# Optimization experiments

Hardware: AMD Instinct MI355X
Metric: run time of the kernel (lower is better)

Reference implementation:

```python
import jax, jax.numpy as jnp
import numpy as np

B, S, E, H, VS, VT = 128, 256, 512, 512, 32000, 32000


def _lstm_layer(x, mask, Wih, Whh, bih, bhh):
    # x: (S,B,E_in), mask: (S,B) bool. PyTorch gate order i,f,g,o.
    h0 = jnp.zeros((x.shape[1], Whh.shape[1]), x.dtype)
    c0 = h0
    def step(carry, inp):
        h, c = carry
        xt, mt = inp
        g = xt @ Wih.T + h @ Whh.T + bih + bhh
        i, f, gg, o = jnp.split(g, 4, axis=-1)
        i = jax.nn.sigmoid(i); f = jax.nn.sigmoid(f)
        gg = jnp.tanh(gg); o = jax.nn.sigmoid(o)
        c_new = f * c + i * gg
        h_new = o * jnp.tanh(c_new)
        m = mt[:, None]
        h2 = jnp.where(m, h_new, h)
        c2 = jnp.where(m, c_new, c)
        return (h2, c2), jnp.where(m, h_new, 0.0)  # pad_packed zero-pads
    (hT, cT), ys = jax.lax.scan(step, (h0, c0), (x, mask))
    return ys, cT


def setup_inputs() -> dict:
    key = jax.random.key(0)
    ks = jax.random.split(key, 32)
    def w(k, shape, fan_in):
        bound = 1.0 / np.sqrt(fan_in)
        return jax.random.uniform(k, shape, jnp.float32, -bound, bound)
    src_tokens = jax.random.randint(ks[0], (B, S), 0, VS)
    src_lens = jnp.sort(jax.random.randint(ks[1], (B,), S // 2, S + 1))[::-1]
    src_lens = src_lens.at[0].set(S)  # pack_padded expects descending, max = S
    trg_tokens = jax.random.randint(ks[2], (B,), 0, VT)
    inp = {
        'src_tokens': src_tokens, 'src_lens': src_lens, 'trg_tokens': trg_tokens,
        'src_emb': jax.random.normal(ks[3], (VS, E), jnp.float32),
        'trg_emb': jax.random.normal(ks[4], (VT, E), jnp.float32),
        'enc_Wih0': w(ks[5], (4 * H, E), H), 'enc_Whh0': w(ks[6], (4 * H, H), H),
        'enc_bih0': w(ks[7], (4 * H,), H), 'enc_bhh0': w(ks[8], (4 * H,), H),
        'enc_Wih1': w(ks[9], (4 * H, H), H), 'enc_Whh1': w(ks[10], (4 * H, H), H),
        'enc_bih1': w(ks[11], (4 * H,), H), 'enc_bhh1': w(ks[12], (4 * H,), H),
        'dec_Wih': w(ks[13], (4 * H, E + H), H), 'dec_Whh': w(ks[14], (4 * H, H), H),
        'dec_bih': w(ks[15], (4 * H,), H), 'dec_bhh': w(ks[16], (4 * H,), H),
        'W_init': w(ks[17], (H, 2 * H), 2 * H), 'b_init': w(ks[18], (H,), 2 * H),
        'W_hid': w(ks[19], (H, 2 * H), 2 * H), 'b_hid': w(ks[20], (H,), 2 * H),
        'W_out': w(ks[21], (VT, H), H), 'b_out': w(ks[22], (VT,), H),
    }
    return inp


def reference(src_tokens, src_lens, trg_tokens, src_emb, trg_emb,
              enc_Wih0, enc_Whh0, enc_bih0, enc_bhh0,
              enc_Wih1, enc_Whh1, enc_bih1, enc_bhh1,
              dec_Wih, dec_Whh, dec_bih, dec_bhh,
              W_init, b_init, W_hid, b_hid, W_out, b_out):
    # ---- encode ----
    x = src_emb[src_tokens]                       # (B,S,E)
    x = jnp.transpose(x, (1, 0, 2))               # (S,B,E)
    mask = jnp.arange(S)[:, None] < src_lens[None, :]  # (S,B)
    y0, c0f = _lstm_layer(x, mask, enc_Wih0, enc_Whh0, enc_bih0, enc_bhh0)
    y1, c1f = _lstm_layer(y0, mask, enc_Wih1, enc_Whh1, enc_bih1, enc_bhh1)
    src_states = jnp.transpose(y1, (1, 0, 2))     # (B,S,H)
    # final cell states (num_layers,B,H) -> (B, num_layers*H)
    final_cells = jnp.concatenate([c0f, c1f], axis=-1)  # (B,2H)
    c_dec = final_cells @ W_init.T + b_init       # (B,H)
    h_dec = jnp.tanh(c_dec)
    # ---- one decoder step ----
    emb_t = trg_emb[trg_tokens]                   # (B,E)
    vec = jnp.concatenate([emb_t, jnp.zeros((B, H), emb_t.dtype)], axis=-1)
    g = vec @ dec_Wih.T + h_dec @ dec_Whh.T + dec_bih + dec_bhh
    i, f, gg, o = jnp.split(g, 4, axis=-1)
    c = jax.nn.sigmoid(f) * c_dec + jax.nn.sigmoid(i) * jnp.tanh(gg)
    h = jax.nn.sigmoid(o) * jnp.tanh(c)           # (B,H)
    # ---- masked dot attention ----
    scores = jnp.einsum('bsh,bh->bs', src_states, h)
    smask = jnp.arange(S)[None, :] < src_lens[:, None]
    scores = jnp.where(smask, scores, -jnp.inf)
    attw = jax.nn.softmax(scores, axis=-1)
    context = jnp.einsum('bs,bsh->bh', attw, src_states)
    attn_vec = jnp.concatenate([h, context], axis=-1) @ W_hid.T + b_hid
    logits = attn_vec @ W_out.T + b_out
    prd_token = jnp.argmax(logits, axis=-1)       # softmax is monotone
    return context, h, prd_token
```

## Files before the change

### kernel.cpp

```cpp
#include <hip/hip_runtime.h>
#include <stdint.h>


typedef _Float16 f16;
typedef f16 f16x8 __attribute__((ext_vector_type(8)));
typedef float f32x4 __attribute__((ext_vector_type(4)));

#define LOSCALE 2048.0f
#define LOINV   (1.0f/2048.0f)

#define B_  128
#define S_  256
#define H_  512

__device__ __forceinline__ uint16_t hbits(f16 h){ union{ f16 f; uint16_t u; } c; c.f=h; return c.u; }

__device__ __forceinline__ uint32_t split_ph2(float x){
  f16 h = (f16)x;
  float r = (x - (float)h) * LOSCALE;
  return (uint32_t)hbits(h) | ((uint32_t)hbits((f16)r) << 16);
}
__device__ __forceinline__ float ph2val(uint32_t p){
  union{ uint16_t u; f16 f; } a, b; a.u = (uint16_t)p; b.u = (uint16_t)(p>>16);
  return (float)a.f + (float)b.f * LOINV;
}

__device__ __forceinline__ void pack_hi_lo(const uint4& a, const uint4& b, uint4& hi, uint4& lo){
  hi = make_uint4((a.x & 0xffffu) | (a.y << 16),
                  (a.z & 0xffffu) | (a.w << 16),
                  (b.x & 0xffffu) | (b.y << 16),
                  (b.z & 0xffffu) | (b.w << 16));
  lo = make_uint4((a.x >> 16) | (a.y & 0xffff0000u),
                  (a.z >> 16) | (a.w & 0xffff0000u),
                  (b.x >> 16) | (b.y & 0xffff0000u),
                  (b.z >> 16) | (b.w & 0xffff0000u));
}

__device__ __forceinline__ void split_pack8(const float* x, uint4& hi, uint4& lo){
  uint16_t h[8], l[8];
#pragma unroll
  for (int e = 0; e < 8; ++e) {
    f16 hh = (f16)x[e];
    float r = (x[e] - (float)hh) * LOSCALE;
    h[e] = hbits(hh); l[e] = hbits((f16)r);
  }
  hi = make_uint4((uint32_t)h[0]|((uint32_t)h[1]<<16), (uint32_t)h[2]|((uint32_t)h[3]<<16),
                  (uint32_t)h[4]|((uint32_t)h[5]<<16), (uint32_t)h[6]|((uint32_t)h[7]<<16));
  lo = make_uint4((uint32_t)l[0]|((uint32_t)l[1]<<16), (uint32_t)l[2]|((uint32_t)l[3]<<16),
                  (uint32_t)l[4]|((uint32_t)l[5]<<16), (uint32_t)l[6]|((uint32_t)l[7]<<16));
}

__device__ __forceinline__ f32x4 mfma16(uint4 a, uint4 b, f32x4 c){
  return __builtin_amdgcn_mfma_f32_16x16x32_f16(
      __builtin_bit_cast(f16x8, a), __builtin_bit_cast(f16x8, b), c, 0, 0, 0);
}

__device__ __forceinline__ float sigm(float x){ return 1.0f/(1.0f + expf(-x)); }
__device__ __forceinline__ float fsigm(float x){ return 1.0f/(1.0f + __expf(-x)); }
__device__ __forceinline__ float ftanh(float x){
  float ax = fabsf(x);
  float e = __expf(-2.0f*ax);
  float r = (1.0f - e)/(1.0f + e);
  return copysignf(r, x);
}

__global__ __launch_bounds__(256) void k_embed_src(const int* __restrict__ tok,
    const float* __restrict__ emb, uint32_t* __restrict__ out)
{
  const size_t total = (size_t)S_ * B_ * H_;
  for (size_t i = (size_t)blockIdx.x*256 + threadIdx.x; i < total; i += (size_t)gridDim.x*256) {
    int e = (int)(i & (H_-1)); int row = (int)(i >> 9);
    int b = row & (B_-1), s = row >> 7;
    int t = tok[b*S_ + s];
    out[i] = split_ph2(emb[(size_t)t*H_ + e]);
  }
}

__global__ __launch_bounds__(256) void k_embed_trg(const int* __restrict__ tok,
    const float* __restrict__ emb, uint32_t* __restrict__ out)
{
  int i = blockIdx.x*256 + threadIdx.x;
  int e = i & (H_-1), b = i >> 9;
  int t = tok[b];
  out[i] = split_ph2(emb[(size_t)t*H_ + e]);
}

__global__ __launch_bounds__(256,2) void k_gemm(
    const uint32_t* __restrict__ A, int lda,
    const void* __restrict__ W, int ldw, int bsplit,
    const float* __restrict__ b0, const float* __restrict__ b1,
    float* __restrict__ C, int N, int K, int addC)
{
  __shared__ uint8_t sm[65536];
  const int tid = threadIdx.x;
  const int lane = tid & 63, wv = tid >> 6;
  const int wm = wv >> 1, wn = wv & 1;
  const int bn0 = blockIdx.x * 128, bm0 = blockIdx.y * 128;

  const int srow = tid >> 1;
  const int skh  = (tid & 1) * 32;
  const int smt  = srow >> 4, sr = srow & 15, skt = tid & 1;

  f32x4 acc0[4][4], acc1[4][4];
#pragma unroll
  for (int i = 0; i < 4; ++i)
#pragma unroll
    for (int j = 0; j < 4; ++j) { acc0[i][j] = (f32x4){0,0,0,0}; acc1[i][j] = (f32x4){0,0,0,0}; }

  for (int k0 = 0; k0 < K; k0 += 64) {
    __syncthreads();
    {
      const uint32_t* ap = A + (size_t)(bm0 + srow) * lda + (k0 + skh);
      uint4 q[8];
#pragma unroll
      for (int e = 0; e < 8; ++e) q[e] = *(const uint4*)(ap + e*4);
#pragma unroll
      for (int kg = 0; kg < 4; ++kg) {
        uint4 hi, lo; pack_hi_lo(q[2*kg], q[2*kg+1], hi, lo);
        uint8_t* dst = sm + (size_t)(smt*2 + skt)*2048 + (size_t)(sr + 16*kg)*16;
        *(uint4*)dst = hi; *(uint4*)(dst + 1024) = lo;
      }
    }
    if (bsplit) {
      const uint32_t* wp = (const uint32_t*)W + (size_t)(bn0 + srow) * ldw + (k0 + skh);
      uint4 q[8];
#pragma unroll
      for (int e = 0; e < 8; ++e) q[e] = *(const uint4*)(wp + e*4);
#pragma unroll
      for (int kg = 0; kg < 4; ++kg) {
        uint4 hi, lo; pack_hi_lo(q[2*kg], q[2*kg+1], hi, lo);
        uint8_t* dst = sm + 32768 + (size_t)(smt*2 + skt)*2048 + (size_t)(sr + 16*kg)*16;
        *(uint4*)dst = hi; *(uint4*)(dst + 1024) = lo;
      }
    } else {
      const float* wp = (const float*)W + (size_t)(bn0 + srow) * ldw + (k0 + skh);
      float xs[32];
#pragma unroll
      for (int e = 0; e < 8; ++e) { float4 v = *(const float4*)(wp + e*4);
        xs[e*4+0]=v.x; xs[e*4+1]=v.y; xs[e*4+2]=v.z; xs[e*4+3]=v.w; }
#pragma unroll
      for (int kg = 0; kg < 4; ++kg) {
        uint4 hi, lo; split_pack8(xs + kg*8, hi, lo);
        uint8_t* dst = sm + 32768 + (size_t)(smt*2 + skt)*2048 + (size_t)(sr + 16*kg)*16;
        *(uint4*)dst = hi; *(uint4*)(dst + 1024) = lo;
      }
    }
    __syncthreads();

#pragma unroll
    for (int kt = 0; kt < 2; ++kt) {
      uint4 ah[4], al[4];
#pragma unroll
      for (int i = 0; i < 4; ++i) {
        const uint8_t* p = sm + (size_t)(((wm*4+i)*2 + kt))*2048 + lane*16;
        ah[i] = *(const uint4*)p; al[i] = *(const uint4*)(p + 1024);
      }
#pragma unroll
      for (int j = 0; j < 4; ++j) {
        const uint8_t* p = sm + 32768 + (size_t)(((wn*4+j)*2 + kt))*2048 + lane*16;
        uint4 bh = *(const uint4*)p;
        uint4 bl = *(const uint4*)(p + 1024);
#pragma unroll
        for (int i = 0; i < 4; ++i) {
          acc0[i][j] = mfma16(ah[i], bh, acc0[i][j]);
          acc1[i][j] = mfma16(al[i], bh, acc1[i][j]);
          acc1[i][j] = mfma16(ah[i], bl, acc1[i][j]);
        }
      }
    }
  }

#pragma unroll
  for (int i = 0; i < 4; ++i) {
    int row0 = bm0 + (wm*4+i)*16 + ((lane>>4)<<2);
#pragma unroll
    for (int j = 0; j < 4; ++j) {
      int col = bn0 + (wn*4+j)*16 + (lane & 15);
      float bias = 0.f;
      if (b0) bias += b0[col];
      if (b1) bias += b1[col];
      f32x4 v = acc0[i][j] + acc1[i][j] * LOINV;
#pragma unroll
      for (int r = 0; r < 4; ++r) {
        size_t idx = (size_t)(row0 + r) * N + col;
        float out = v[r] + bias;
        if (addC) out += C[idx];
        C[idx] = out;
      }
    }
  }
}

__global__ __launch_bounds__(256,1) void k_lstm(
    const float* __restrict__ Whh,
    const float* __restrict__ xg,
    const int*  __restrict__ lens,
    uint32_t* __restrict__ hbuf,
    float* __restrict__ cbuf,
    uint32_t* __restrict__ ybuf,
    uint32_t* __restrict__ flags,
    int s0, int nsteps)
{
  __shared__ uint64_t htile64[4096];
  __shared__ float gates_lds[1024];
  uint8_t* htile = (uint8_t*)htile64;
  const int tid = threadIdx.x, lane = tid & 63, wv = tid >> 6;
  const int bg = blockIdx.x & 7, hs = blockIdx.x >> 3;
  const int row = lane & 15, qh = lane >> 4;

  uint4 wbh[16], wbl[16];
  {
    const float* wrow = Whh + (size_t)(wv*512 + hs*16 + row) * 512 + qh*8;
#pragma unroll
    for (int kt = 0; kt < 16; ++kt) {
      float xs[8];
      float4 v0 = *(const float4*)(wrow + kt*32);
      float4 v1 = *(const float4*)(wrow + kt*32 + 4);
      xs[0]=v0.x; xs[1]=v0.y; xs[2]=v0.z; xs[3]=v0.w;
      xs[4]=v1.x; xs[5]=v1.y; xs[6]=v1.z; xs[7]=v1.w;
      split_pack8(xs, wbh[kt], wbl[kt]);
    }
  }

  const int b_l = tid >> 4, uu = tid & 15;
  const int bglob = bg*16 + b_l;
  const size_t bgoff = (size_t)bg*8192;
  const int oct_p = hs*2 + (uu >> 3);
  const size_t widx = (size_t)b_l*512 + (size_t)(uu & 1)*256
                    + (size_t)((oct_p ^ b_l) << 2) + (size_t)((uu & 7) >> 1);
  float c_reg = cbuf[(size_t)bglob*512 + hs*16 + uu];
  float h_reg;
  {
    size_t ib = (size_t)(s0 & 1)*65536 + bgoff + (size_t)b_l*512
              + (size_t)((oct_p ^ b_l) << 2) + (size_t)((uu & 7) >> 1);
    uint32_t hiw = hbuf[ib];
    uint32_t low = hbuf[ib + 256];
    int sh = (uu & 1) * 16;
    union{ uint16_t u; f16 f; } ch, cl;
    ch.u = (uint16_t)(hiw >> sh); cl.u = (uint16_t)(low >> sh);
    h_reg = (float)ch.f + (float)cl.f * LOINV;
  }
  const int len_b = lens[bglob];
  __syncthreads();

  for (int sl = 0; sl < nsteps; ++sl) {
    const int s = s0 + sl;

    const float* xgp = xg + ((size_t)sl*128 + bglob)*2048 + hs*16 + uu;
    float xv0 = xgp[0], xv1 = xgp[512], xv2 = xgp[1024], xv3 = xgp[1536];

    if (sl > 0) {
      if (wv == 0) {
        const uint32_t* fp = flags + bg*32 + (lane & 31);
        while (1) {
          uint32_t f = __hip_atomic_load(fp, __ATOMIC_RELAXED, __HIP_MEMORY_SCOPE_SYSTEM);
          if (__all((int)(f >= (uint32_t)s))) break;
          __builtin_amdgcn_s_sleep(1);
        }
      }
      __syncthreads();
    }

    {
      const uint64_t* src = (const uint64_t*)(hbuf + (size_t)(s & 1)*65536 + bgoff);
      uint64_t v[16];
#pragma unroll
      for (int e = 0; e < 16; ++e)
        v[e] = __hip_atomic_load(src + tid + e*256, __ATOMIC_RELAXED, __HIP_MEMORY_SCOPE_SYSTEM);
#pragma unroll
      for (int e = 0; e < 16; ++e)
        htile64[tid + e*256] = v[e];
    }
    __syncthreads();

    f32x4 a0 = (f32x4){0,0,0,0}, a1 = (f32x4){0,0,0,0}, a2 = (f32x4){0,0,0,0};
    const uint8_t* hrowp = htile + (size_t)row*2048;
#pragma unroll
    for (int kt = 0; kt < 16; ++kt) {
      int oct = kt*4 + qh;
      const uint8_t* p = hrowp + (((oct ^ row)) << 4);
      uint4 ah = *(const uint4*)p;
      uint4 al = *(const uint4*)(p + 1024);
      a0 = mfma16(ah, wbh[kt], a0);
      a1 = mfma16(al, wbh[kt], a1);
      a2 = mfma16(ah, wbl[kt], a2);
    }
    {
      int col = lane & 15, rbase = (lane >> 4) << 2;
#pragma unroll
      for (int r = 0; r < 4; ++r)
        gates_lds[(size_t)(wv*16 + rbase + r)*16 + col] = a0[r] + (a1[r] + a2[r])*LOINV;
    }
    __syncthreads();

    float gi = gates_lds[(size_t)(0*16 + b_l)*16 + uu] + xv0;
    float gf = gates_lds[(size_t)(1*16 + b_l)*16 + uu] + xv1;
    float gg = gates_lds[(size_t)(2*16 + b_l)*16 + uu] + xv2;
    float go = gates_lds[(size_t)(3*16 + b_l)*16 + uu] + xv3;
    float cn = fsigm(gf)*c_reg + fsigm(gi)*ftanh(gg);
    float hn = fsigm(go)*ftanh(cn);
    bool m = (s < len_b);
    c_reg = m ? cn : c_reg;
    h_reg = m ? hn : h_reg;

    uint32_t p = split_ph2(h_reg);
    uint32_t pp = __shfl_xor(p, 1);
    uint32_t wword = (uu & 1) ? ((pp >> 16) | (p & 0xffff0000u))
                              : ((p & 0xffffu) | (pp << 16));
    __hip_atomic_store(hbuf + (size_t)((s + 1) & 1)*65536 + bgoff + widx,
                       wword, __ATOMIC_RELAXED, __HIP_MEMORY_SCOPE_SYSTEM);
    asm volatile("s_waitcnt vmcnt(0)" ::: "memory");
    __syncthreads();
    if (tid == 0)
      __hip_atomic_store(flags + bg*32 + hs, (uint32_t)(s + 1),
                         __ATOMIC_RELAXED, __HIP_MEMORY_SCOPE_SYSTEM);
    ybuf[(size_t)s*65536 + (size_t)bglob*512 + hs*16 + uu] = m ? p : 0u;
  }
  cbuf[(size_t)bglob*512 + hs*16 + uu] = c_reg;
}

__global__ __launch_bounds__(256) void k_pack2(const float* __restrict__ a,
    const float* __restrict__ b, uint32_t* __restrict__ out)
{
  int i = blockIdx.x*256 + threadIdx.x;
  int bb = i >> 10, k = i & 1023;
  float x = (k < 512) ? a[(size_t)bb*512 + k] : b[(size_t)bb*512 + k - 512];
  out[i] = split_ph2(x);
}

__global__ __launch_bounds__(256) void k_pack1(const float* __restrict__ a,
    uint32_t* __restrict__ out)
{ int i = blockIdx.x*256 + threadIdx.x; out[i] = split_ph2(a[i]); }

__global__ __launch_bounds__(256) void k_tanh_split(const float* __restrict__ c,
    uint32_t* __restrict__ hp)
{ int i = blockIdx.x*256 + threadIdx.x; hp[i] = split_ph2(tanhf(c[i])); }

__global__ __launch_bounds__(256) void k_dec_cell(const float* __restrict__ g,
    const float* __restrict__ cdec, float* __restrict__ hout, float* __restrict__ dh)
{
  int i = blockIdx.x*256 + threadIdx.x;
  int b = i >> 9, u = i & 511;
  const float* gb = g + (size_t)b*2048;
  float c = sigm(gb[512 + u])*cdec[i] + sigm(gb[u])*tanhf(gb[1024 + u]);
  float h = sigm(gb[1536 + u])*tanhf(c);
  hout[i] = h; dh[i] = h;
}

__global__ __launch_bounds__(256) void k_attn(const uint32_t* __restrict__ y1,
    const float* __restrict__ h, const int* __restrict__ lens,
    float* __restrict__ ctx, float* __restrict__ dctx)
{
  __shared__ float hsh[512];
  __shared__ float sc[256];
  __shared__ float red[8];
  const int b = blockIdx.x, tid = threadIdx.x, lane = tid & 63, wv = tid >> 6;
  hsh[tid]       = h[(size_t)b*512 + tid];
  hsh[tid + 256] = h[(size_t)b*512 + tid + 256];
  const int len = lens[b];
  __syncthreads();

  for (int it = 0; it < 64; ++it) {
    int s = wv*64 + it;
    const uint32_t* yp = y1 + ((size_t)s*128 + b)*512 + lane*8;
    uint4 p0 = *(const uint4*)yp, p1 = *(const uint4*)(yp + 4);
    uint32_t pv[8] = {p0.x,p0.y,p0.z,p0.w,p1.x,p1.y,p1.z,p1.w};
    float d = 0.f;
#pragma unroll
    for (int e = 0; e < 8; ++e) d += ph2val(pv[e]) * hsh[lane*8 + e];
    for (int off = 32; off; off >>= 1) d += __shfl_xor(d, off);
    if (lane == 0) sc[s] = d;
  }
  __syncthreads();

  float v = (tid < len) ? sc[tid] : -INFINITY;
  float mx = v;
  for (int off = 32; off; off >>= 1) mx = fmaxf(mx, __shfl_xor(mx, off));
  if (lane == 0) red[wv] = mx;
  __syncthreads();
  mx = fmaxf(fmaxf(red[0], red[1]), fmaxf(red[2], red[3]));
  float e = (tid < len) ? expf(v - mx) : 0.f;
  float ssum = e;
  for (int off = 32; off; off >>= 1) ssum += __shfl_xor(ssum, off);
  if (lane == 0) red[4 + wv] = ssum;
  __syncthreads();
  float tot = red[4] + red[5] + red[6] + red[7];
  __syncthreads();
  sc[tid] = e / tot;
  __syncthreads();

  float acc0 = 0.f, acc1 = 0.f;
  for (int s = 0; s < 256; ++s) {
    float w = sc[s];
    const uint32_t* yp = y1 + ((size_t)s*128 + b)*512;
    acc0 += w * ph2val(yp[tid]);
    acc1 += w * ph2val(yp[tid + 256]);
  }
  ctx [(size_t)b*512 + tid]       = acc0;  ctx [(size_t)b*512 + tid + 256] = acc1;
  dctx[(size_t)b*512 + tid]       = acc0;  dctx[(size_t)b*512 + tid + 256] = acc1;
}

__global__ __launch_bounds__(256) void k_argmax(const float* __restrict__ logits,
    float* __restrict__ out)
{
  __shared__ float bv[256];
  __shared__ int   bi[256];
  const int b = blockIdx.x, tid = threadIdx.x;
  const float* L = logits + (size_t)b*32000;
  float best = -INFINITY; int idx = 0;
  for (int i = tid; i < 32000; i += 256) {
    float v = L[i];
    if (v > best) { best = v; idx = i; }
  }
  bv[tid] = best; bi[tid] = idx;
  __syncthreads();
  for (int sft = 128; sft; sft >>= 1) {
    if (tid < sft) {
      if (bv[tid+sft] > bv[tid] || (bv[tid+sft] == bv[tid] && bi[tid+sft] < bi[tid])) {
        bv[tid] = bv[tid+sft]; bi[tid] = bi[tid+sft];
      }
    }
    __syncthreads();
  }
  if (tid == 0) out[b] = (float)bi[0];
}

extern "C" void kernel_launch(void* const* d_in, const int* in_sizes, int n_in,
                              void* d_out, int out_size, void* d_ws, size_t ws_size,
                              hipStream_t stream)
{
  (void)in_sizes; (void)n_in; (void)out_size;
  const int*   src_tokens = (const int*)  d_in[0];
  const int*   src_lens   = (const int*)  d_in[1];
  const int*   trg_tokens = (const int*)  d_in[2];
  const float* src_emb    = (const float*)d_in[3];
  const float* trg_emb    = (const float*)d_in[4];
  const float* Wih0 = (const float*)d_in[5];
  const float* Whh0 = (const float*)d_in[6];
  const float* bih0 = (const float*)d_in[7];
  const float* bhh0 = (const float*)d_in[8];
  const float* Wih1 = (const float*)d_in[9];
  const float* Whh1 = (const float*)d_in[10];
  const float* bih1 = (const float*)d_in[11];
  const float* bhh1 = (const float*)d_in[12];
  const float* dWih = (const float*)d_in[13];
  const float* dWhh = (const float*)d_in[14];
  const float* dbih = (const float*)d_in[15];
  const float* dbhh = (const float*)d_in[16];
  const float* Winit= (const float*)d_in[17];
  const float* binit= (const float*)d_in[18];
  const float* Whid = (const float*)d_in[19];
  const float* bhid = (const float*)d_in[20];
  const float* Wout = (const float*)d_in[21];
  const float* bout = (const float*)d_in[22];

  uint8_t* ws = (uint8_t*)d_ws;
  constexpr size_t MBs = 1ull << 20;
  constexpr size_t OFF_AP    = 0;
  constexpr size_t OFF_Y0    = 64*MBs;
  constexpr size_t OFF_XG    = 128*MBs;
  constexpr size_t OFF_HBUF  = 192*MBs;
  constexpr size_t OFF_CB0   = OFF_HBUF  + 512*1024;
  constexpr size_t OFF_CB1   = OFF_CB0   + 256*1024;
  constexpr size_t OFF_FLG   = OFF_CB1   + 256*1024;
  constexpr size_t OFF_PK    = OFF_FLG   + 4096;
  constexpr size_t OFF_CDEC  = OFF_PK    + 512*1024;
  constexpr size_t OFF_HDECP = OFF_CDEC  + 256*1024;
  constexpr size_t OFF_EMBP  = OFF_HDECP + 256*1024;
  constexpr size_t OFF_G     = OFF_EMBP  + 256*1024;
  constexpr size_t OFF_HDEC2 = OFF_G     + 1*MBs;
  constexpr size_t OFF_CTX   = OFF_HDEC2 + 256*1024;
  constexpr size_t OFF_AVEC  = OFF_CTX   + 256*1024;
  constexpr size_t OFF_AVECP = OFF_AVEC  + 256*1024;
  constexpr size_t OFF_LOG   = OFF_AVECP + 256*1024;
  constexpr size_t OFF_WP0   = OFF_LOG   + 16*MBs;
  constexpr size_t OFF_WP1   = OFF_WP0   + 4*MBs;
  constexpr size_t WS_NEED_WP = OFF_WP1 + 4*MBs;

  uint32_t* Ap    = (uint32_t*)(ws + OFF_AP);
  uint32_t* Y0    = (uint32_t*)(ws + OFF_Y0);
  uint32_t* Y1    = (uint32_t*)(ws + OFF_AP);
  float*    Xg    = (float*)   (ws + OFF_XG);
  uint32_t* hbuf  = (uint32_t*)(ws + OFF_HBUF);
  float*    cb0   = (float*)   (ws + OFF_CB0);
  float*    cb1   = (float*)   (ws + OFF_CB1);
  uint32_t* flg   = (uint32_t*)(ws + OFF_FLG);
  uint32_t* pk    = (uint32_t*)(ws + OFF_PK);
  float*    cdec  = (float*)   (ws + OFF_CDEC);
  uint32_t* hdecp = (uint32_t*)(ws + OFF_HDECP);
  uint32_t* embp  = (uint32_t*)(ws + OFF_EMBP);
  float*    g     = (float*)   (ws + OFF_G);
  float*    hdec2 = (float*)   (ws + OFF_HDEC2);
  float*    ctx   = (float*)   (ws + OFF_CTX);
  float*    avec  = (float*)   (ws + OFF_AVEC);
  uint32_t* avecp = (uint32_t*)(ws + OFF_AVECP);
  float*    logit = (float*)   (ws + OFF_LOG);
  uint32_t* Wp0   = (uint32_t*)(ws + OFF_WP0);
  uint32_t* Wp1   = (uint32_t*)(ws + OFF_WP1);
  float*    dout  = (float*)   d_out;

  const bool useWp = (ws_size >= WS_NEED_WP);

  if (useWp) {
    k_pack1<<<4096, 256, 0, stream>>>(Wih0, Wp0);
    k_pack1<<<4096, 256, 0, stream>>>(Wih1, Wp1);
  }

  hipMemsetAsync(flg,  0, 1024, stream);
  hipMemsetAsync(hbuf, 0, 2*65536*4, stream);
  hipMemsetAsync(cb0,  0, 65536*4, stream);
  k_embed_src<<<2048, 256, 0, stream>>>(src_tokens, src_emb, Ap);
  for (int c = 0; c < 4; ++c) {
    int s0 = c * 64;
    if (useWp)
      k_gemm<<<dim3(16, 64), 256, 0, stream>>>(Ap + (size_t)s0*128*512, 512,
          Wp0, 512, 1, bih0, bhh0, Xg, 2048, 512, 0);
    else
      k_gemm<<<dim3(16, 64), 256, 0, stream>>>(Ap + (size_t)s0*128*512, 512,
          Wih0, 512, 0, bih0, bhh0, Xg, 2048, 512, 0);
    k_lstm<<<256, 256, 0, stream>>>(Whh0, Xg, src_lens, hbuf, cb0, Y0, flg, s0, 64);
  }
  hipMemsetAsync(flg,  0, 1024, stream);
  hipMemsetAsync(hbuf, 0, 2*65536*4, stream);
  hipMemsetAsync(cb1,  0, 65536*4, stream);
  for (int c = 0; c < 4; ++c) {
    int s0 = c * 64;
    if (useWp)
      k_gemm<<<dim3(16, 64), 256, 0, stream>>>(Y0 + (size_t)s0*128*512, 512,
          Wp1, 512, 1, bih1, bhh1, Xg, 2048, 512, 0);
    else
      k_gemm<<<dim3(16, 64), 256, 0, stream>>>(Y0 + (size_t)s0*128*512, 512,
          Wih1, 512, 0, bih1, bhh1, Xg, 2048, 512, 0);
    k_lstm<<<256, 256, 0, stream>>>(Whh1, Xg, src_lens, hbuf, cb1, Y1, flg, s0, 64);
  }

  k_pack2<<<512, 256, 0, stream>>>(cb0, cb1, pk);
  k_gemm<<<dim3(4, 1), 256, 0, stream>>>(pk, 1024, Winit, 1024, 0, binit, nullptr,
      cdec, 512, 1024, 0);
  k_tanh_split<<<256, 256, 0, stream>>>(cdec, hdecp);

  k_embed_trg<<<256, 256, 0, stream>>>(trg_tokens, trg_emb, embp);
  k_gemm<<<dim3(16, 1), 256, 0, stream>>>(embp, 512, dWih, 1024, 0, dbih, dbhh,
      g, 2048, 512, 0);
  k_gemm<<<dim3(16, 1), 256, 0, stream>>>(hdecp, 512, dWhh, 512, 0, nullptr, nullptr,
      g, 2048, 512, 1);
  k_dec_cell<<<256, 256, 0, stream>>>(g, cdec, hdec2, dout + 65536);

  k_attn<<<128, 256, 0, stream>>>(Y1, hdec2, src_lens, ctx, dout);

  k_pack2<<<512, 256, 0, stream>>>(hdec2, ctx, pk);
  k_gemm<<<dim3(4, 1), 256, 0, stream>>>(pk, 1024, Whid, 1024, 0, bhid, nullptr,
      avec, 512, 1024, 0);
  k_pack1<<<256, 256, 0, stream>>>(avec, avecp);
  k_gemm<<<dim3(250, 1), 256, 0, stream>>>(avecp, 512, Wout, 512, 0, bout, nullptr,
      logit, 32000, 512, 0);
  k_argmax<<<128, 256, 0, stream>>>(logit, dout + 131072);
}
```

Baseline: 2.688 ms.

## Pre-tile operands into MFMA fragment layout and stream via global_load_lds

Adds a fragment-major 'fl' layout with separate hi/lo planes, used by the source embedding, the packed input weights, the LSTM output Y and W_out. A new GEMM kernel moves tiles straight from global memory into LDS with global_load_lds and no repacking. The LSTM hidden-state load is split into two halves so the second half's LDS stores overlap the first half's MFMAs. Attention is rewritten to read the new Y layout, and W_out is now packed on every call, which adds extra traffic to that path.

New measurement: 2.775 ms. 3.2% more time.

```diff
diff --git a/kernel.cpp b/kernel.cpp
--- a/kernel.cpp
+++ b/kernel.cpp
@@ -64,15 +64,36 @@
   return copysignf(r, x);
 }
 
-__global__ __launch_bounds__(256) void k_embed_src(const int* __restrict__ tok,
+__device__ __forceinline__ uint32_t plane_word(uint32_t p, uint32_t pp, int odd){
+  return odd ? ((pp >> 16) | (p & 0xffff0000u))
+             : ((p & 0xffffu) | (pp << 16));
+}
+
+__device__ __forceinline__ size_t fl_idx(int row, int k){
+  return (size_t)(k >> 5) * 4096 + (size_t)(row >> 4) * 512 + (size_t)(k & 1) * 256
+       + (size_t)((k >> 3) & 3) * 64 + (size_t)(row & 15) * 4 + (size_t)((k & 7) >> 1);
+}
+
+__device__ __forceinline__ void gload_lds16(const uint32_t* gbase, uint32_t* lbase, int lane){
+#if __has_builtin(__builtin_amdgcn_global_load_lds)
+  __builtin_amdgcn_global_load_lds(
+      (const __attribute__((address_space(1))) uint32_t*)(gbase + lane*4),
+      (__attribute__((address_space(3))) uint32_t*)lbase, 16, 0, 0);
+#else
+  *(uint4*)(lbase + lane*4) = *(const uint4*)(gbase + lane*4);
+#endif
+}
+
+__global__ __launch_bounds__(256) void k_embed_src_fl(const int* __restrict__ tok,
     const float* __restrict__ emb, uint32_t* __restrict__ out)
 {
   const size_t total = (size_t)S_ * B_ * H_;
   for (size_t i = (size_t)blockIdx.x*256 + threadIdx.x; i < total; i += (size_t)gridDim.x*256) {
-    int e = (int)(i & (H_-1)); int row = (int)(i >> 9);
-    int b = row & (B_-1), s = row >> 7;
+    int s = (int)(i >> 16), b = (int)((i >> 9) & 127), k = (int)(i & 511);
     int t = tok[b*S_ + s];
-    out[i] = split_ph2(emb[(size_t)t*H_ + e]);
+    uint32_t p = split_ph2(emb[(size_t)t*H_ + k]);
+    uint32_t pp = __shfl_xor(p, 1);
+    out[(size_t)s*65536 + fl_idx(b, k)] = plane_word(p, pp, k & 1);
   }
 }
 
@@ -85,9 +106,104 @@
   out[i] = split_ph2(emb[(size_t)t*H_ + e]);
 }
 
+__global__ __launch_bounds__(256) void k_packW(const float* __restrict__ W,
+    uint32_t* __restrict__ out)
+{
+  int i = blockIdx.x*256 + threadIdx.x;
+  int n = i >> 9, k = i & 511;
+  uint32_t p = split_ph2(W[i]);
+  uint32_t pp = __shfl_xor(p, 1);
+  out[(size_t)(n >> 7)*65536 + fl_idx(n & 127, k)] = plane_word(p, pp, k & 1);
+}
+
+__global__ __launch_bounds__(256) void k_packAfl(const float* __restrict__ a,
+    uint32_t* __restrict__ out)
+{
+  int i = blockIdx.x*256 + threadIdx.x;
+  int b = i >> 9, k = i & 511;
+  uint32_t p = split_ph2(a[i]);
+  uint32_t pp = __shfl_xor(p, 1);
+  out[fl_idx(b, k)] = plane_word(p, pp, k & 1);
+}
+
+__global__ __launch_bounds__(256,2) void k_gemm_fl(
+    const uint32_t* __restrict__ Afl,
+    const uint32_t* __restrict__ Wfl,
+    const float* __restrict__ b0, const float* __restrict__ b1,
+    float* __restrict__ C, int N, int addC)
+{
+  __shared__ uint8_t sm[65536];
+  const int tid = threadIdx.x, lane = tid & 63, wv = tid >> 6;
+  const int wm = wv >> 1, wn = wv & 1;
+  const int bn0 = blockIdx.x * 128, bm0 = blockIdx.y * 128;
+  const uint32_t* Ab = Afl + (size_t)blockIdx.y * 65536;
+  const uint32_t* Wb = Wfl + (size_t)blockIdx.x * 65536;
+
+  f32x4 acc0[4][4], acc1[4][4];
+#pragma unroll
+  for (int i = 0; i < 4; ++i)
+#pragma unroll
+    for (int j = 0; j < 4; ++j) { acc0[i][j] = (f32x4){0,0,0,0}; acc1[i][j] = (f32x4){0,0,0,0}; }
+
+  for (int it = 0; it < 8; ++it) {
+    __syncthreads();
+    {
+      const uint32_t* gsrc = (wv < 2 ? Ab : Wb) + (size_t)it*8192 + (size_t)(wv & 1)*4096;
+      uint32_t* lb = (uint32_t*)(sm + (size_t)wv*16384);
+#pragma unroll
+      for (int e = 0; e < 16; ++e)
+        gload_lds16(gsrc + e*256, lb + e*256, lane);
+    }
+    asm volatile("s_waitcnt vmcnt(0)" ::: "memory");
+    __syncthreads();
+
+#pragma unroll
+    for (int kt = 0; kt < 2; ++kt) {
+      uint4 ah[4], al[4];
+#pragma unroll
+      for (int i = 0; i < 4; ++i) {
+        const uint8_t* p = sm + (size_t)(kt*8 + wm*4 + i)*2048 + lane*16;
+        ah[i] = *(const uint4*)p; al[i] = *(const uint4*)(p + 1024);
+      }
+#pragma unroll
+      for (int j = 0; j < 4; ++j) {
+        const uint8_t* p = sm + 32768 + (size_t)(kt*8 + wn*4 + j)*2048 + lane*16;
+        uint4 bh = *(const uint4*)p;
+        uint4 bl = *(const uint4*)(p + 1024);
+#pragma unroll
+        for (int i = 0; i < 4; ++i) {
+          acc0[i][j] = mfma16(ah[i], bh, acc0[i][j]);
+          acc1[i][j] = mfma16(al[i], bh, acc1[i][j]);
+          acc1[i][j] = mfma16(ah[i], bl, acc1[i][j]);
+        }
+      }
+    }
+  }
+
+#pragma unroll
+  for (int i = 0; i < 4; ++i) {
+    int row0 = bm0 + (wm*4+i)*16 + ((lane>>4)<<2);
+#pragma unroll
+    for (int j = 0; j < 4; ++j) {
+      int col = bn0 + (wn*4+j)*16 + (lane & 15);
+      float bias = 0.f;
+      if (b0) bias += b0[col];
+      if (b1) bias += b1[col];
+      f32x4 v = acc0[i][j] + acc1[i][j] * LOINV;
+#pragma unroll
+      for (int r = 0; r < 4; ++r) {
+        size_t idx = (size_t)(row0 + r) * N + col;
+        float out = v[r] + bias;
+        if (addC) out += C[idx];
+        C[idx] = out;
+      }
+    }
+  }
+}
+
 __global__ __launch_bounds__(256,2) void k_gemm(
     const uint32_t* __restrict__ A, int lda,
-    const void* __restrict__ W, int ldw, int bsplit,
+    const float* __restrict__ W, int ldw,
     const float* __restrict__ b0, const float* __restrict__ b1,
     float* __restrict__ C, int N, int K, int addC)
 {
@@ -121,19 +237,8 @@
         *(uint4*)dst = hi; *(uint4*)(dst + 1024) = lo;
       }
     }
-    if (bsplit) {
-      const uint32_t* wp = (const uint32_t*)W + (size_t)(bn0 + srow) * ldw + (k0 + skh);
-      uint4 q[8];
-#pragma unroll
-      for (int e = 0; e < 8; ++e) q[e] = *(const uint4*)(wp + e*4);
-#pragma unroll
-      for (int kg = 0; kg < 4; ++kg) {
-        uint4 hi, lo; pack_hi_lo(q[2*kg], q[2*kg+1], hi, lo);
-        uint8_t* dst = sm + 32768 + (size_t)(smt*2 + skt)*2048 + (size_t)(sr + 16*kg)*16;
-        *(uint4*)dst = hi; *(uint4*)(dst + 1024) = lo;
-      }
-    } else {
-      const float* wp = (const float*)W + (size_t)(bn0 + srow) * ldw + (k0 + skh);
+    {
+      const float* wp = W + (size_t)(bn0 + srow) * ldw + (k0 + skh);
       float xs[32];
 #pragma unroll
       for (int e = 0; e < 8; ++e) { float4 v = *(const float4*)(wp + e*4);
@@ -241,6 +346,15 @@
     h_reg = (float)ch.f + (float)cl.f * LOINV;
   }
   const int len_b = lens[bglob];
+  const size_t yfl = (size_t)(hs >> 1)*4096 + (size_t)bg*512 + (size_t)(uu & 1)*256
+                   + (size_t)((((hs & 1) << 1) | (uu >> 3)))*64 + (size_t)b_l*4
+                   + (size_t)((uu & 7) >> 1);
+  int sidx[8];
+#pragma unroll
+  for (int e = 0; e < 8; ++e) {
+    int j = e*256 + tid; int r2 = j >> 7, sub = j & 127;
+    sidx[e] = r2*256 + ((sub >> 6) << 7) + (sub & 63);
+  }
   __syncthreads();
 
   for (int sl = 0; sl < nsteps; ++sl) {
@@ -261,22 +375,41 @@
       __syncthreads();
     }
 
-    {
-      const uint64_t* src = (const uint64_t*)(hbuf + (size_t)(s & 1)*65536 + bgoff);
-      uint64_t v[16];
-#pragma unroll
-      for (int e = 0; e < 16; ++e)
-        v[e] = __hip_atomic_load(src + tid + e*256, __ATOMIC_RELAXED, __HIP_MEMORY_SCOPE_SYSTEM);
-#pragma unroll
-      for (int e = 0; e < 16; ++e)
-        htile64[tid + e*256] = v[e];
-    }
-    __syncthreads();
+    const uint64_t* src = (const uint64_t*)(hbuf + (size_t)(s & 1)*65536 + bgoff);
+    uint64_t v0[8], v1[8];
+#pragma unroll
+    for (int e = 0; e < 8; ++e)
+      v0[e] = __hip_atomic_load(src + sidx[e], __ATOMIC_RELAXED, __HIP_MEMORY_SCOPE_SYSTEM);
+#pragma unroll
+    for (int e = 0; e < 8; ++e)
+      v1[e] = __hip_atomic_load(src + sidx[e] + 64, __ATOMIC_RELAXED, __HIP_MEMORY_SCOPE_SYSTEM);
+#pragma unroll
+    for (int e = 0; e < 8; ++e)
+      htile64[sidx[e]] = v0[e];
+    asm volatile("s_waitcnt lgkmcnt(0)" ::: "memory");
+    __builtin_amdgcn_s_barrier();
+    __builtin_amdgcn_sched_barrier(0);
 
     f32x4 a0 = (f32x4){0,0,0,0}, a1 = (f32x4){0,0,0,0}, a2 = (f32x4){0,0,0,0};
     const uint8_t* hrowp = htile + (size_t)row*2048;
 #pragma unroll
-    for (int kt = 0; kt < 16; ++kt) {
+    for (int kt = 0; kt < 8; ++kt) {
+      int oct = kt*4 + qh;
+      const uint8_t* p = hrowp + (((oct ^ row)) << 4);
+      uint4 ah = *(const uint4*)p;
+      uint4 al = *(const uint4*)(p + 1024);
+      a0 = mfma16(ah, wbh[kt], a0);
+      a1 = mfma16(al, wbh[kt], a1);
+      a2 = mfma16(ah, wbl[kt], a2);
+    }
+#pragma unroll
+    for (int e = 0; e < 8; ++e)
+      htile64[sidx[e] + 64] = v1[e];
+    asm volatile("s_waitcnt lgkmcnt(0)" ::: "memory");
+    __builtin_amdgcn_s_barrier();
+    __builtin_amdgcn_sched_barrier(0);
+#pragma unroll
+    for (int kt = 8; kt < 16; ++kt) {
       int oct = kt*4 + qh;
       const uint8_t* p = hrowp + (((oct ^ row)) << 4);
       uint4 ah = *(const uint4*)p;
@@ -305,8 +438,7 @@
 
     uint32_t p = split_ph2(h_reg);
     uint32_t pp = __shfl_xor(p, 1);
-    uint32_t wword = (uu & 1) ? ((pp >> 16) | (p & 0xffff0000u))
-                              : ((p & 0xffffu) | (pp << 16));
+    uint32_t wword = plane_word(p, pp, uu & 1);
     __hip_atomic_store(hbuf + (size_t)((s + 1) & 1)*65536 + bgoff + widx,
                        wword, __ATOMIC_RELAXED, __HIP_MEMORY_SCOPE_SYSTEM);
     asm volatile("s_waitcnt vmcnt(0)" ::: "memory");
@@ -314,7 +446,7 @@
     if (tid == 0)
       __hip_atomic_store(flags + bg*32 + hs, (uint32_t)(s + 1),
                          __ATOMIC_RELAXED, __HIP_MEMORY_SCOPE_SYSTEM);
-    ybuf[(size_t)s*65536 + (size_t)bglob*512 + hs*16 + uu] = m ? p : 0u;
+    ybuf[(size_t)s*65536 + yfl] = m ? wword : 0u;
   }
   cbuf[(size_t)bglob*512 + hs*16 + uu] = c_reg;
 }
@@ -327,10 +459,6 @@
   float x = (k < 512) ? a[(size_t)bb*512 + k] : b[(size_t)bb*512 + k - 512];
   out[i] = split_ph2(x);
 }
-
-__global__ __launch_bounds__(256) void k_pack1(const float* __restrict__ a,
-    uint32_t* __restrict__ out)
-{ int i = blockIdx.x*256 + threadIdx.x; out[i] = split_ph2(a[i]); }
 
 __global__ __launch_bounds__(256) void k_tanh_split(const float* __restrict__ c,
     uint32_t* __restrict__ hp)
@@ -360,14 +488,24 @@
   const int len = lens[b];
   __syncthreads();
 
+  const size_t lanebase = (size_t)(lane >> 2)*4096 + (size_t)(b >> 4)*512
+                        + (size_t)(lane & 3)*64 + (size_t)(b & 15)*4;
   for (int it = 0; it < 64; ++it) {
     int s = wv*64 + it;
-    const uint32_t* yp = y1 + ((size_t)s*128 + b)*512 + lane*8;
-    uint4 p0 = *(const uint4*)yp, p1 = *(const uint4*)(yp + 4);
-    uint32_t pv[8] = {p0.x,p0.y,p0.z,p0.w,p1.x,p1.y,p1.z,p1.w};
+    const uint32_t* yb = y1 + (size_t)s*65536 + lanebase;
+    uint4 hw = *(const uint4*)yb;
+    uint4 lw = *(const uint4*)(yb + 256);
+    int k0 = lane*8;
+    uint32_t hws[4] = {hw.x,hw.y,hw.z,hw.w}, lws[4] = {lw.x,lw.y,lw.z,lw.w};
     float d = 0.f;
 #pragma unroll
-    for (int e = 0; e < 8; ++e) d += ph2val(pv[e]) * hsh[lane*8 + e];
+    for (int w = 0; w < 4; ++w) {
+      union{uint16_t u; f16 f;} h0,h1,l0,l1;
+      h0.u=(uint16_t)hws[w]; h1.u=(uint16_t)(hws[w]>>16);
+      l0.u=(uint16_t)lws[w]; l1.u=(uint16_t)(lws[w]>>16);
+      d += ((float)h0.f + (float)l0.f*LOINV) * hsh[k0 + 2*w]
+         + ((float)h1.f + (float)l1.f*LOINV) * hsh[k0 + 2*w + 1];
+    }
     for (int off = 32; off; off >>= 1) d += __shfl_xor(d, off);
     if (lane == 0) sc[s] = d;
   }
@@ -389,12 +527,23 @@
   sc[tid] = e / tot;
   __syncthreads();
 
+  const int u0 = tid, u1 = tid + 256;
+  const size_t bu0 = (size_t)(u0 >> 5)*4096 + (size_t)(b >> 4)*512
+                   + (size_t)((u0 >> 3) & 3)*64 + (size_t)(b & 15)*4 + (size_t)((u0 & 7) >> 1);
+  const size_t bu1 = (size_t)(u1 >> 5)*4096 + (size_t)(b >> 4)*512
+                   + (size_t)((u1 >> 3) & 3)*64 + (size_t)(b & 15)*4 + (size_t)((u1 & 7) >> 1);
+  const int sh = (tid & 1) * 16;
   float acc0 = 0.f, acc1 = 0.f;
   for (int s = 0; s < 256; ++s) {
     float w = sc[s];
-    const uint32_t* yp = y1 + ((size_t)s*128 + b)*512;
-    acc0 += w * ph2val(yp[tid]);
-    acc1 += w * ph2val(yp[tid + 256]);
+    const uint32_t* yb = y1 + (size_t)s*65536;
+    uint32_t hi0 = yb[bu0], lo0 = yb[bu0 + 256];
+    uint32_t hi1 = yb[bu1], lo1 = yb[bu1 + 256];
+    union{uint16_t u; f16 f;} a,b2,c2,d2;
+    a.u =(uint16_t)(hi0 >> sh); b2.u=(uint16_t)(lo0 >> sh);
+    c2.u=(uint16_t)(hi1 >> sh); d2.u=(uint16_t)(lo1 >> sh);
+    acc0 += w*((float)a.f  + (float)b2.f*LOINV);
+    acc1 += w*((float)c2.f + (float)d2.f*LOINV);
   }
   ctx [(size_t)b*512 + tid]       = acc0;  ctx [(size_t)b*512 + tid + 256] = acc1;
   dctx[(size_t)b*512 + tid]       = acc0;  dctx[(size_t)b*512 + tid + 256] = acc1;
@@ -429,7 +578,7 @@
                               void* d_out, int out_size, void* d_ws, size_t ws_size,
                               hipStream_t stream)
 {
-  (void)in_sizes; (void)n_in; (void)out_size;
+  (void)in_sizes; (void)n_in; (void)out_size; (void)ws_size;
   const int*   src_tokens = (const int*)  d_in[0];
   const int*   src_lens   = (const int*)  d_in[1];
   const int*   trg_tokens = (const int*)  d_in[2];
@@ -473,14 +622,12 @@
   constexpr size_t OFF_AVEC  = OFF_CTX   + 256*1024;
   constexpr size_t OFF_AVECP = OFF_AVEC  + 256*1024;
   constexpr size_t OFF_LOG   = OFF_AVECP + 256*1024;
-  constexpr size_t OFF_WP0   = OFF_LOG   + 16*MBs;
-  constexpr size_t OFF_WP1   = OFF_WP0   + 4*MBs;
-  constexpr size_t WS_NEED_WP = OFF_WP1 + 4*MBs;
 
   uint32_t* Ap    = (uint32_t*)(ws + OFF_AP);
   uint32_t* Y0    = (uint32_t*)(ws + OFF_Y0);
   uint32_t* Y1    = (uint32_t*)(ws + OFF_AP);
   float*    Xg    = (float*)   (ws + OFF_XG);
+  uint32_t* WoutF = (uint32_t*)(ws + OFF_XG);
   uint32_t* hbuf  = (uint32_t*)(ws + OFF_HBUF);
   float*    cb0   = (float*)   (ws + OFF_CB0);
   float*    cb1   = (float*)   (ws + OFF_CB1);
@@ -495,29 +642,21 @@
   float*    avec  = (float*)   (ws + OFF_AVEC);
   uint32_t* avecp = (uint32_t*)(ws + OFF_AVECP);
   float*    logit = (float*)   (ws + OFF_LOG);
-  uint32_t* Wp0   = (uint32_t*)(ws + OFF_WP0);
-  uint32_t* Wp1   = (uint32_t*)(ws + OFF_WP1);
+  uint32_t* Wp0   = (uint32_t*)(ws + OFF_LOG);
+  uint32_t* Wp1   = (uint32_t*)(ws + OFF_LOG + 4*MBs);
   float*    dout  = (float*)   d_out;
 
-  const bool useWp = (ws_size >= WS_NEED_WP);
-
-  if (useWp) {
-    k_pack1<<<4096, 256, 0, stream>>>(Wih0, Wp0);
-    k_pack1<<<4096, 256, 0, stream>>>(Wih1, Wp1);
-  }
+  k_packW<<<4096, 256, 0, stream>>>(Wih0, Wp0);
+  k_packW<<<4096, 256, 0, stream>>>(Wih1, Wp1);
 
   hipMemsetAsync(flg,  0, 1024, stream);
   hipMemsetAsync(hbuf, 0, 2*65536*4, stream);
   hipMemsetAsync(cb0,  0, 65536*4, stream);
-  k_embed_src<<<2048, 256, 0, stream>>>(src_tokens, src_emb, Ap);
+  k_embed_src_fl<<<2048, 256, 0, stream>>>(src_tokens, src_emb, Ap);
   for (int c = 0; c < 4; ++c) {
     int s0 = c * 64;
-    if (useWp)
-      k_gemm<<<dim3(16, 64), 256, 0, stream>>>(Ap + (size_t)s0*128*512, 512,
-          Wp0, 512, 1, bih0, bhh0, Xg, 2048, 512, 0);
-    else
-      k_gemm<<<dim3(16, 64), 256, 0, stream>>>(Ap + (size_t)s0*128*512, 512,
-          Wih0, 512, 0, bih0, bhh0, Xg, 2048, 512, 0);
+    k_gemm_fl<<<dim3(16, 64), 256, 0, stream>>>(Ap + (size_t)s0*65536,
+        Wp0, bih0, bhh0, Xg, 2048, 0);
     k_lstm<<<256, 256, 0, stream>>>(Whh0, Xg, src_lens, hbuf, cb0, Y0, flg, s0, 64);
   }
   hipMemsetAsync(flg,  0, 1024, stream);
@@ -525,34 +664,32 @@
   hipMemsetAsync(cb1,  0, 65536*4, stream);
   for (int c = 0; c < 4; ++c) {
     int s0 = c * 64;
-    if (useWp)
-      k_gemm<<<dim3(16, 64), 256, 0, stream>>>(Y0 + (size_t)s0*128*512, 512,
-          Wp1, 512, 1, bih1, bhh1, Xg, 2048, 512, 0);
-    else
-      k_gemm<<<dim3(16, 64), 256, 0, stream>>>(Y0 + (size_t)s0*128*512, 512,
-          Wih1, 512, 0, bih1, bhh1, Xg, 2048, 512, 0);
+    k_gemm_fl<<<dim3(16, 64), 256, 0, stream>>>(Y0 + (size_t)s0*65536,
+        Wp1, bih1, bhh1, Xg, 2048, 0);
     k_lstm<<<256, 256, 0, stream>>>(Whh1, Xg, src_lens, hbuf, cb1, Y1, flg, s0, 64);
   }
 
+  k_packW<<<64000, 256, 0, stream>>>(Wout, WoutF);
+
   k_pack2<<<512, 256, 0, stream>>>(cb0, cb1, pk);
-  k_gemm<<<dim3(4, 1), 256, 0, stream>>>(pk, 1024, Winit, 1024, 0, binit, nullptr,
+  k_gemm<<<dim3(4, 1), 256, 0, stream>>>(pk, 1024, Winit, 1024, binit, nullptr,
       cdec, 512, 1024, 0);
   k_tanh_split<<<256, 256, 0, stream>>>(cdec, hdecp);
 
   k_embed_trg<<<256, 256, 0, stream>>>(trg_tokens, trg_emb, embp);
-  k_gemm<<<dim3(16, 1), 256, 0, stream>>>(embp, 512, dWih, 1024, 0, dbih, dbhh,
+  k_gemm<<<dim3(16, 1), 256, 0, stream>>>(embp, 512, dWih, 1024, dbih, dbhh,
       g, 2048, 512, 0);
-  k_gemm<<<dim3(16, 1), 256, 0, stream>>>(hdecp, 512, dWhh, 512, 0, nullptr, nullptr,
+  k_gemm<<<dim3(16, 1), 256, 0, stream>>>(hdecp, 512, dWhh, 512, nullptr, nullptr,
       g, 2048, 512, 1);
   k_dec_cell<<<256, 256, 0, stream>>>(g, cdec, hdec2, dout + 65536);
 
   k_attn<<<128, 256, 0, stream>>>(Y1, hdec2, src_lens, ctx, dout);
 
   k_pack2<<<512, 256, 0, stream>>>(hdec2, ctx, pk);
-  k_gemm<<<dim3(4, 1), 256, 0, stream>>>(pk, 1024, Whid, 1024, 0, bhid, nullptr,
+  k_gemm<<<dim3(4, 1), 256, 0, stream>>>(pk, 1024, Whid, 1024, bhid, nullptr,
       avec, 512, 1024, 0);
-  k_pack1<<<256, 256, 0, stream>>>(avec, avecp);
-  k_gemm<<<dim3(250, 1), 256, 0, stream>>>(avecp, 512, Wout, 512, 0, bout, nullptr,
-      logit, 32000, 512, 0);
+  k_packAfl<<<256, 256, 0, stream>>>(avec, avecp);
+  k_gemm_fl<<<dim3(250, 1), 256, 0, stream>>>(avecp, WoutF, bout, nullptr,
+      logit, 32000, 0);
   k_argmax<<<128, 256, 0, stream>>>(logit, dout + 131072);
 }
```
